# Optimization experiments

Measured on AMD Instinct MI355X. Metric: run time of the kernel, lower is better.

The kernel has to match this reference:

```python
import jax, jax.numpy as jnp
import numpy as np

P, PDIM, Q, N = 100000, 64, 64, 32768


def setup_inputs() -> dict:
    key = jax.random.key(0)
    k0, k1, k2, k3 = jax.random.split(key, 4)
    x0 = jax.random.normal(k0, (P, PDIM), dtype=jnp.float32)
    x0 = x0.at[:, 0].set(1.0)  # _init_params: x0[:, 0] = 1.0
    ell = jnp.array([2.6279, 2.63, 2.6295], dtype=jnp.float32)
    poses = jax.random.normal(k1, (Q, 12), dtype=jnp.float32)
    d = jax.random.randint(k2, (N,), 0, P)
    w = jax.random.randint(k3, (N,), 0, Q)
    return {"x0": x0, "ell": ell, "poses": poses, "d": d, "w": w}


def reference(x0, ell, poses, d, w):
    # E = exp(diag(ell)) elementwise: exp(ell_k) on the diagonal, exp(0)=1 off-diagonal
    # (faithful to torch.exp(torch.diag(ell)) in the original).
    E = jnp.exp(jnp.diag(ell))  # [3, 3]
    Rs = poses.reshape(-1, 3, 4)[:, :3, :3]  # [Q, 3, 3] rotations
    # tr(R1 @ E @ R2^T) for all (i, j) pairs, batched instead of Q*Q python loop
    tr_term = jnp.einsum('iab,bc,jac->ij', Rs, E, Rs)  # [Q, Q]
    v0 = jnp.exp(-0.5 * (jnp.trace(E) - tr_term))  # [Q, Q]
    # normalize_rows(x0)
    xn = x0 / jnp.sqrt(jnp.einsum('ij,ij->i', x0, x0))[:, None]  # [P, p]
    X = xn[d]   # [N, p] embedding lookup
    W = v0[w]   # [N, Q] embedding lookup
    V = X[:, :, None] * W[:, None, :]  # [N, p, Q] outer product
    return V.reshape(V.shape[0], -1)   # [N, p*Q]
```

## Files before the change

### kernel.cpp

```cpp
#include <hip/hip_runtime.h>
#include <math.h>

__global__ void compute_v0_kernel(const float* __restrict__ ell,
                                  const float* __restrict__ poses,
                                  float* __restrict__ v0) {
    int idx = blockIdx.x * blockDim.x + threadIdx.x;
    int i = idx >> 6;
    int j = idx & 63;
    float e0 = expf(ell[0]), e1 = expf(ell[1]), e2 = expf(ell[2]);
    float trE = e0 + e1 + e2;
    const float* Ri = poses + i * 12;
    const float* Rj = poses + j * 12;
    float tr = 0.f;
#pragma unroll
    for (int a = 0; a < 3; ++a) {
        float ri0 = Ri[a * 4 + 0], ri1 = Ri[a * 4 + 1], ri2 = Ri[a * 4 + 2];
        float rj0 = Rj[a * 4 + 0], rj1 = Rj[a * 4 + 1], rj2 = Rj[a * 4 + 2];
        float si = ri0 + ri1 + ri2;
        float sj = rj0 + rj1 + rj2;
        tr += si * sj + ri0 * rj0 * (e0 - 1.f) + ri1 * rj1 * (e1 - 1.f) +
              ri2 * rj2 * (e2 - 1.f);
    }
    float arg = -0.5f * (trE - tr);
    v0[idx] = expf(fminf(arg, 88.0f));
}

__global__ __launch_bounds__(256) void outer_kernel(
    const float* __restrict__ x0,
    const int* __restrict__ d,
    const int* __restrict__ w,
    const float* __restrict__ v0,
    float* __restrict__ out) {
    __shared__ float xs[64];
    __shared__ float vs[64];
    __shared__ float s_inv;

    const int n = blockIdx.x;
    const int t = threadIdx.x;
    const int dn = d[n];
    const int wn = w[n];

    if (t < 64) {
        float val = x0[(size_t)dn * 64 + t];
        xs[t] = val;
        float sq = val * val;
#pragma unroll
        for (int off = 32; off > 0; off >>= 1) sq += __shfl_down(sq, off, 64);
        if (t == 0) s_inv = rsqrtf(sq);
    } else if (t < 128) {
        vs[t - 64] = v0[wn * 64 + (t - 64)];
    }
    __syncthreads();

    const float inv = s_inv;
    const float4 vq = ((const float4*)vs)[t & 15];
    float4* out4 = (float4*)(out + (size_t)n * 4096);

#pragma unroll
    for (int i = 0; i < 4; ++i) {
        int p = i * 16 + (t >> 4);
        float xv = xs[p] * inv;
        float4 o;
        o.x = xv * vq.x;
        o.y = xv * vq.y;
        o.z = xv * vq.z;
        o.w = xv * vq.w;
        out4[i * 256 + t] = o;
    }
}

extern "C" void kernel_launch(void* const* d_in, const int* in_sizes, int n_in,
                              void* d_out, int out_size, void* d_ws, size_t ws_size,
                              hipStream_t stream) {
    const float* x0    = (const float*)d_in[0];
    const float* ell   = (const float*)d_in[1];
    const float* poses = (const float*)d_in[2];
    const int*   d     = (const int*)d_in[3];
    const int*   w     = (const int*)d_in[4];
    float* out = (float*)d_out;
    float* v0  = (float*)d_ws;

    const int N = in_sizes[3];

    compute_v0_kernel<<<16, 256, 0, stream>>>(ell, poses, v0);
    outer_kernel<<<N, 256, 0, stream>>>(x0, d, w, v0, out);
}
```

Baseline: 544.0 us.

## Process multiple rows per block with register prefetch and optional prenormalization

The outer-product kernel now handles 16 output rows per block instead of one. It double-buffers the next row's gathered x and v0 values in registers while writing the current row, and broadcasts x with wavefront shuffles instead of shared memory and a barrier. A separate kernel can normalize all of x0 into workspace ahead of time when the workspace is large enough, which removes the per-row reduction. That kernel normalizes every one of the P rows, though only the N gathered rows are ever used, which adds extra memory traffic.

```diff
diff --git a/kernel.cpp b/kernel.cpp
--- a/kernel.cpp
+++ b/kernel.cpp
@@ -25,47 +25,75 @@
     v0[idx] = expf(fminf(arg, 88.0f));
 }
 
+__global__ __launch_bounds__(256) void normalize_kernel(
+    const float* __restrict__ x0, float* __restrict__ xn, int P) {
+    int row = blockIdx.x * 4 + (threadIdx.x >> 6);
+    if (row >= P) return;
+    int l = threadIdx.x & 63;
+    float v = x0[(size_t)row * 64 + l];
+    float sq = v * v;
+#pragma unroll
+    for (int off = 32; off > 0; off >>= 1) sq += __shfl_xor(sq, off, 64);
+    xn[(size_t)row * 64 + l] = v * rsqrtf(sq);
+}
+
+template <int ROWS, bool PRENORM>
 __global__ __launch_bounds__(256) void outer_kernel(
-    const float* __restrict__ x0,
+    const float* __restrict__ xsrc,
     const int* __restrict__ d,
     const int* __restrict__ w,
     const float* __restrict__ v0,
     float* __restrict__ out) {
-    __shared__ float xs[64];
-    __shared__ float vs[64];
-    __shared__ float s_inv;
+    const int t = threadIdx.x;
+    const int lane = t & 63;
+    const long n0 = (long)blockIdx.x * ROWS;
 
-    const int n = blockIdx.x;
-    const int t = threadIdx.x;
-    const int dn = d[n];
-    const int wn = w[n];
+    float xv[2];
+    float4 v4[2];
 
-    if (t < 64) {
-        float val = x0[(size_t)dn * 64 + t];
-        xs[t] = val;
-        float sq = val * val;
+    {
+        int dn = d[n0], wn = w[n0];
+        float x = xsrc[(size_t)dn * 64 + lane];
+        if (!PRENORM) {
+            float sq = x * x;
 #pragma unroll
-        for (int off = 32; off > 0; off >>= 1) sq += __shfl_down(sq, off, 64);
-        if (t == 0) s_inv = rsqrtf(sq);
-    } else if (t < 128) {
-        vs[t - 64] = v0[wn * 64 + (t - 64)];
+            for (int off = 32; off > 0; off >>= 1) sq += __shfl_xor(sq, off, 64);
+            x *= rsqrtf(sq);
+        }
+        xv[0] = x;
+        v4[0] = ((const float4*)(v0 + wn * 64))[t & 15];
     }
-    __syncthreads();
-
-    const float inv = s_inv;
-    const float4 vq = ((const float4*)vs)[t & 15];
-    float4* out4 = (float4*)(out + (size_t)n * 4096);
 
 #pragma unroll
-    for (int i = 0; i < 4; ++i) {
-        int p = i * 16 + (t >> 4);
-        float xv = xs[p] * inv;
-        float4 o;
-        o.x = xv * vq.x;
-        o.y = xv * vq.y;
-        o.z = xv * vq.z;
-        o.w = xv * vq.w;
-        out4[i * 256 + t] = o;
+    for (int r = 0; r < ROWS; ++r) {
+        const int cur = r & 1;
+        const int nxt = cur ^ 1;
+        if (r + 1 < ROWS) {
+            int dn = d[n0 + r + 1], wn = w[n0 + r + 1];
+            float x = xsrc[(size_t)dn * 64 + lane];
+            if (!PRENORM) {
+                float sq = x * x;
+#pragma unroll
+                for (int off = 32; off > 0; off >>= 1)
+                    sq += __shfl_xor(sq, off, 64);
+                x *= rsqrtf(sq);
+            }
+            xv[nxt] = x;
+            v4[nxt] = ((const float4*)(v0 + wn * 64))[t & 15];
+        }
+
+        const float4 vq = v4[cur];
+        float4* out4 = (float4*)(out + (size_t)(n0 + r) * 4096);
+#pragma unroll
+        for (int i = 0; i < 4; ++i) {
+            float xi = __shfl(xv[cur], i * 16 + (t >> 4), 64);
+            float4 o;
+            o.x = xi * vq.x;
+            o.y = xi * vq.y;
+            o.z = xi * vq.z;
+            o.w = xi * vq.w;
+            out4[i * 256 + t] = o;
+        }
     }
 }
 
@@ -81,7 +109,28 @@
     float* v0  = (float*)d_ws;
 
     const int N = in_sizes[3];
+    const int P = in_sizes[0] / 64;
 
     compute_v0_kernel<<<16, 256, 0, stream>>>(ell, poses, v0);
-    outer_kernel<<<N, 256, 0, stream>>>(x0, d, w, v0, out);
+
+    const size_t xn_bytes = (size_t)P * 64 * sizeof(float);
+    const bool prenorm = ws_size >= 16384 + xn_bytes;
+    float* xn = (float*)((char*)d_ws + 16384);
+
+    if (prenorm) {
+        normalize_kernel<<<(P + 3) / 4, 256, 0, stream>>>(x0, xn, P);
+    }
+
+    constexpr int ROWS = 16;
+    if ((N % ROWS) == 0) {
+        if (prenorm)
+            outer_kernel<ROWS, true><<<N / ROWS, 256, 0, stream>>>(xn, d, w, v0, out);
+        else
+            outer_kernel<ROWS, false><<<N / ROWS, 256, 0, stream>>>(x0, d, w, v0, out);
+    } else {
+        if (prenorm)
+            outer_kernel<1, true><<<N, 256, 0, stream>>>(xn, d, w, v0, out);
+        else
+            outer_kernel<1, false><<<N, 256, 0, stream>>>(x0, d, w, v0, out);
+    }
 }
```

Result: slower. 564.2 us (+3.7%).

## Prenormalize x0, batch rows per block with prefetch, use nontemporal stores

Applied to the files above, without the earlier changes.

Adds a separate pass that normalizes every row of x0 into workspace, so the outer-product kernel only gathers precomputed rows. Each block now handles several output rows, with register prefetch of the next gathered x and v0 values, and writes output with nontemporal stores and no shared memory or barrier. A fallback kernel that uses wavefront shuffles is used when the workspace is too small. The extra normalization pass reads and writes the whole x0 table, even though only the gathered rows are needed.

```diff
diff --git a/kernel.cpp b/kernel.cpp
--- a/kernel.cpp
+++ b/kernel.cpp
@@ -1,5 +1,7 @@
 #include <hip/hip_runtime.h>
 #include <math.h>
+
+typedef float vf4 __attribute__((ext_vector_type(4)));
 
 __global__ void compute_v0_kernel(const float* __restrict__ ell,
                                   const float* __restrict__ poses,
@@ -25,47 +27,84 @@
     v0[idx] = expf(fminf(arg, 88.0f));
 }
 
-__global__ __launch_bounds__(256) void outer_kernel(
+__global__ __launch_bounds__(256) void normalize_kernel(
+    const float* __restrict__ x0, float* __restrict__ xn, int P) {
+    int row = blockIdx.x * 16 + (threadIdx.x >> 4);
+    if (row >= P) return;
+    int g = threadIdx.x & 15;
+    vf4 v = ((const vf4*)(x0 + (size_t)row * 64))[g];
+    float sq = v.x * v.x + v.y * v.y + v.z * v.z + v.w * v.w;
+#pragma unroll
+    for (int off = 8; off > 0; off >>= 1) sq += __shfl_xor(sq, off, 64);
+    float inv = rsqrtf(sq);
+    vf4 o = {v.x * inv, v.y * inv, v.z * inv, v.w * inv};
+    ((vf4*)(xn + (size_t)row * 64))[g] = o;
+}
+
+template <int ROWS, int DEPTH>
+__global__ __launch_bounds__(256, 8) void outer_kernel(
+    const float* __restrict__ xn,
+    const int* __restrict__ d,
+    const int* __restrict__ w,
+    const float* __restrict__ v0,
+    float* __restrict__ out) {
+    const int t = threadIdx.x;
+    const int g16 = t >> 4;
+    const int q4 = t & 15;
+    const long n0 = (long)blockIdx.x * ROWS;
+
+    float xr[ROWS][4];
+    vf4 vr[ROWS];
+
+    auto prefetch = [&](int r) {
+        int dn = d[n0 + r];
+        int wn = w[n0 + r];
+        const float* xp = xn + (size_t)dn * 64 + g16;
+#pragma unroll
+        for (int i = 0; i < 4; ++i) xr[r][i] = xp[i * 16];
+        vr[r] = ((const vf4*)(v0 + wn * 64))[q4];
+    };
+
+    constexpr int PRE = DEPTH < ROWS ? DEPTH : ROWS;
+#pragma unroll
+    for (int r = 0; r < PRE; ++r) prefetch(r);
+
+#pragma unroll
+    for (int r = 0; r < ROWS; ++r) {
+        if (r + PRE < ROWS) prefetch(r + PRE);
+        const vf4 vq = vr[r];
+        vf4* ob = (vf4*)(out + (size_t)(n0 + r) * 4096);
+#pragma unroll
+        for (int i = 0; i < 4; ++i) {
+            float xi = xr[r][i];
+            vf4 o = {xi * vq.x, xi * vq.y, xi * vq.z, xi * vq.w};
+            __builtin_nontemporal_store(o, ob + i * 256 + t);
+        }
+    }
+}
+
+__global__ __launch_bounds__(256, 8) void outer_kernel_fb(
     const float* __restrict__ x0,
     const int* __restrict__ d,
     const int* __restrict__ w,
     const float* __restrict__ v0,
     float* __restrict__ out) {
-    __shared__ float xs[64];
-    __shared__ float vs[64];
-    __shared__ float s_inv;
-
-    const int n = blockIdx.x;
     const int t = threadIdx.x;
-    const int dn = d[n];
-    const int wn = w[n];
-
-    if (t < 64) {
-        float val = x0[(size_t)dn * 64 + t];
-        xs[t] = val;
-        float sq = val * val;
+    const int lane = t & 63;
+    const long n = blockIdx.x;
+    int dn = d[n], wn = w[n];
+    float x = x0[(size_t)dn * 64 + lane];
+    float sq = x * x;
 #pragma unroll
-        for (int off = 32; off > 0; off >>= 1) sq += __shfl_down(sq, off, 64);
-        if (t == 0) s_inv = rsqrtf(sq);
-    } else if (t < 128) {
-        vs[t - 64] = v0[wn * 64 + (t - 64)];
-    }
-    __syncthreads();
-
-    const float inv = s_inv;
-    const float4 vq = ((const float4*)vs)[t & 15];
-    float4* out4 = (float4*)(out + (size_t)n * 4096);
-
+    for (int off = 32; off > 0; off >>= 1) sq += __shfl_xor(sq, off, 64);
+    x *= rsqrtf(sq);
+    vf4 vq = ((const vf4*)(v0 + wn * 64))[t & 15];
+    vf4* ob = (vf4*)(out + (size_t)n * 4096);
 #pragma unroll
     for (int i = 0; i < 4; ++i) {
-        int p = i * 16 + (t >> 4);
-        float xv = xs[p] * inv;
-        float4 o;
-        o.x = xv * vq.x;
-        o.y = xv * vq.y;
-        o.z = xv * vq.z;
-        o.w = xv * vq.w;
-        out4[i * 256 + t] = o;
+        float xi = __shfl(x, i * 16 + (t >> 4), 64);
+        vf4 o = {xi * vq.x, xi * vq.y, xi * vq.z, xi * vq.w};
+        __builtin_nontemporal_store(o, ob + i * 256 + t);
     }
 }
 
@@ -81,7 +120,20 @@
     float* v0  = (float*)d_ws;
 
     const int N = in_sizes[3];
+    const int P = in_sizes[0] / 64;
 
     compute_v0_kernel<<<16, 256, 0, stream>>>(ell, poses, v0);
-    outer_kernel<<<N, 256, 0, stream>>>(x0, d, w, v0, out);
+
+    const size_t xn_bytes = (size_t)P * 64 * sizeof(float);
+    const bool prenorm = ws_size >= 16384 + xn_bytes;
+    float* xn = (float*)((char*)d_ws + 16384);
+
+    constexpr int ROWS = 8;
+    constexpr int DEPTH = 3;
+    if (prenorm && (N % ROWS) == 0) {
+        normalize_kernel<<<(P + 15) / 16, 256, 0, stream>>>(x0, xn, P);
+        outer_kernel<ROWS, DEPTH><<<N / ROWS, 256, 0, stream>>>(xn, d, w, v0, out);
+    } else {
+        outer_kernel_fb<<<N, 256, 0, stream>>>(x0, d, w, v0, out);
+    }
 }
```

New measurement: 562.3 us. 1.03x slower.
